# Optimization experiments

Hardware: AMD Instinct MI355X
Metric: run time of the kernel (lower is better)

## Reference

```python
import jax, jax.numpy as jnp
import numpy as np

K = 20.0          # wavenumber_k
L = 0.01          # grid_spacing_l
_lm = [L ** (i + 1) for i in range(7)]
C1 = jnp.array([[_lm[0], _lm[1]/2, _lm[2]/3, _lm[3]/4],
                [_lm[1]/2, _lm[2]/3, _lm[3]/4, _lm[4]/5],
                [_lm[2]/3, _lm[3]/4, _lm[4]/5, _lm[5]/6],
                [_lm[3]/4, _lm[4]/5, _lm[5]/6, _lm[6]/7]], dtype=jnp.float32)
C2 = jnp.array([[0,0,0,0],[0,0,0,0],[0,0,4*_lm[0],6*_lm[1]],[0,0,6*_lm[1],12*_lm[2]]], dtype=jnp.float32)
C3 = jnp.array([[0,0,0,0],[0,0,0,0],[2*_lm[0],_lm[1],2/3*_lm[2],1/2*_lm[3]],[3*_lm[1],2*_lm[2],3/2*_lm[3],6/5*_lm[4]]], dtype=jnp.float32)
M  = jnp.array([[1,0,0,0],[0,0,1,0],[-3/_lm[1],3/_lm[1],-2/_lm[0],-1/_lm[0]],[2/_lm[2],-2/_lm[2],1/_lm[1],1/_lm[1]]], dtype=jnp.float32)


def setup_inputs() -> dict:
    key = jax.random.key(0)
    x = jax.random.normal(key, (16, 4, 512, 512), dtype=jnp.float32)
    return {"x": x}


def _helmholtz(x):
    # corner views: (B, 4, H-1, W-1)
    tl = x[:, :, :-1, :-1]
    tr = x[:, :, :-1, 1:]
    bl = x[:, :, 1:, :-1]
    br = x[:, :, 1:, 1:]
    # rows replicate the original module exactly (including row_3's use of
    # du_xy_tl twice and du_x_tr); row_4 stacked on last dim.
    row1 = jnp.stack([tl[:, 0], tr[:, 0], tl[:, 2], tr[:, 2]], axis=-1)
    row2 = jnp.stack([bl[:, 0], br[:, 0], bl[:, 2], br[:, 2]], axis=-1)
    row3 = jnp.stack([tl[:, 3], tr[:, 1], tl[:, 3], tr[:, 3]], axis=-1)
    row4 = jnp.stack([bl[:, 1], br[:, 1], bl[:, 3], br[:, 3]], axis=-1)
    Q = jnp.stack([row1, row2, row3, row4], axis=-2)  # (B, H-1, W-1, 4, 4)
    # A = M @ Q @ M^T
    A = jnp.einsum('ij,bhwjk,lk->bhwil', M, Q, M)

    def quad(Cm):
        # sum over all entries of A @ Cm @ A^T, per patch -> (B, H-1, W-1)
        return jnp.einsum('bhwij,jk,bhwlk->bhw', A, Cm, A)

    s1 = jnp.sum(C1)
    s2 = jnp.sum(C2)
    s3 = jnp.sum(C3)
    qC1  = quad(C1)
    qC2  = quad(C2)
    qC3T = quad(C3.T)
    qC3  = quad(C3)
    k2 = K * K
    patch = (s2 * qC1 + s1 * qC2 + (k2 * k2) * s1 * qC1
             + 2.0 * s3 * qC3T + 2.0 * k2 * s1 * qC3 + 2.0 * k2 * s3 * qC1)
    return jnp.mean(patch)


def reference(x):
    return _helmholtz(x)
```

## Files before the change

### kernel.cpp

```cpp
#include <hip/hip_runtime.h>


struct HParams {
    float u0, u1, u2, u3;
    float Hs[4][4];
};

#define ROWS_PER_TILE 8
#define NTILES 64
#define BSIZE 256

__global__ __launch_bounds__(BSIZE) void helm_main(const float* __restrict__ x,
                                                   double* __restrict__ partial,
                                                   HParams P)
{
    const int bid  = blockIdx.x;
    const int b    = bid >> 6;
    const int tile = bid & 63;
    const int h0   = tile * ROWS_PER_TILE;
    const int rend = min(h0 + ROWS_PER_TILE, 511);
    const int t    = threadIdx.x;

    __shared__ float raw[4][512];
    __shared__ float buf[2][5][512];
    __shared__ double wsum[4];

    const float* xb = x + (size_t)b * 4u * 512u * 512u;

    const int c0 = t >> 7;
    const int c1 = 2 + (t >> 7);
    const int q  = t & 127;
    const float4* p0 = (const float4*)(xb + (size_t)c0 * 262144u) + q;
    const float4* p1 = (const float4*)(xb + (size_t)c1 * 262144u) + q;

    double acc = 0.0;

    float4 r0 = p0[(size_t)h0 * 128u];
    float4 r1 = p1[(size_t)h0 * 128u];

    for (int r = h0; r <= rend; ++r) {
        ((float4*)raw[c0])[q] = r0;
        ((float4*)raw[c1])[q] = r1;
        float4 n0 = make_float4(0.f, 0.f, 0.f, 0.f);
        float4 n1 = make_float4(0.f, 0.f, 0.f, 0.f);
        if (r < rend) {
            n0 = p0[(size_t)(r + 1) * 128u];
            n1 = p1[(size_t)(r + 1) * 128u];
        }
        __syncthreads();

        {
            float (*bw)[512] = buf[r & 1];
            #pragma unroll
            for (int k = 0; k < 2; ++k) {
                const int w = t + k * 256;
                const float x0 = raw[0][w];
                const float x1 = raw[1][w];
                const float x2 = raw[2][w];
                const float x3 = raw[3][w];
                bw[0][w] = P.u0 * x0 + P.u2 * x3;
                bw[1][w] = P.u0 * x0 + P.u2 * x1;
                bw[2][w] = P.u1 * x0 + P.u3 * x1;
                bw[3][w] = P.u0 * x2 + P.u2 * x3;
                bw[4][w] = P.u1 * x2 + P.u3 * x3;
            }
        }
        __syncthreads();

        if (r > h0) {
            const float (*bt)[512] = buf[(r - 1) & 1];
            const float (*bb)[512] = buf[r & 1];
            #pragma unroll
            for (int k = 0; k < 2; ++k) {
                const int w = t + k * 256;
                if (w < 511) {
                    const float w0 = bt[0][w]     + bb[2][w];
                    const float w1 = bt[1][w + 1] + bb[2][w + 1];
                    const float w2 = bt[3][w]     + bb[4][w];
                    const float w3 = bt[3][w + 1] + bb[4][w + 1];
                    const float t0 = P.Hs[0][0]*w0 + P.Hs[0][1]*w1 + P.Hs[0][2]*w2 + P.Hs[0][3]*w3;
                    const float t1 = P.Hs[1][0]*w0 + P.Hs[1][1]*w1 + P.Hs[1][2]*w2 + P.Hs[1][3]*w3;
                    const float t2 = P.Hs[2][0]*w0 + P.Hs[2][1]*w1 + P.Hs[2][2]*w2 + P.Hs[2][3]*w3;
                    const float t3 = P.Hs[3][0]*w0 + P.Hs[3][1]*w1 + P.Hs[3][2]*w2 + P.Hs[3][3]*w3;
                    acc += (double)(w0 * t0 + w1 * t1 + w2 * t2 + w3 * t3);
                }
            }
        }
        __syncthreads();

        r0 = n0;
        r1 = n1;
    }

    for (int off = 32; off > 0; off >>= 1)
        acc += __shfl_down(acc, off, 64);
    const int lane = t & 63;
    const int wid  = t >> 6;
    if (lane == 0) wsum[wid] = acc;
    __syncthreads();
    if (t == 0)
        partial[bid] = wsum[0] + wsum[1] + wsum[2] + wsum[3];
}

__global__ __launch_bounds__(BSIZE) void helm_reduce(const double* __restrict__ partial,
                                                     float* __restrict__ out, int n)
{
    __shared__ double wsum[4];
    const int t = threadIdx.x;
    double a = 0.0;
    for (int i = t; i < n; i += BSIZE) a += partial[i];
    for (int off = 32; off > 0; off >>= 1)
        a += __shfl_down(a, off, 64);
    if ((t & 63) == 0) wsum[t >> 6] = a;
    __syncthreads();
    if (t == 0) {
        const double sum = wsum[0] + wsum[1] + wsum[2] + wsum[3];
        out[0] = (float)(sum / (16.0 * 511.0 * 511.0));
    }
}

extern "C" void kernel_launch(void* const* d_in, const int* in_sizes, int n_in,
                              void* d_out, int out_size, void* d_ws, size_t ws_size,
                              hipStream_t stream) {
    const float* x = (const float*)d_in[0];
    float* out     = (float*)d_out;
    double* partial = (double*)d_ws;

    const double L = 0.01;
    double lm[7];
    lm[0] = L;
    for (int i = 1; i < 7; ++i) lm[i] = lm[i - 1] * L;

    double C1[4][4], C2[4][4] = {}, C3[4][4] = {};
    for (int i = 0; i < 4; ++i)
        for (int j = 0; j < 4; ++j)
            C1[i][j] = lm[i + j] / (double)(i + j + 1);
    C2[2][2] = 4.0 * lm[0];  C2[2][3] = 6.0 * lm[1];
    C2[3][2] = 6.0 * lm[1];  C2[3][3] = 12.0 * lm[2];
    C3[2][0] = 2.0 * lm[0];  C3[2][1] = lm[1];
    C3[2][2] = (2.0 / 3.0) * lm[2];  C3[2][3] = 0.5 * lm[3];
    C3[3][0] = 3.0 * lm[1];  C3[3][1] = 2.0 * lm[2];
    C3[3][2] = 1.5 * lm[3];  C3[3][3] = (6.0 / 5.0) * lm[4];

    const double M[4][4] = {
        {1.0, 0.0, 0.0, 0.0},
        {0.0, 0.0, 1.0, 0.0},
        {-3.0 / lm[1], 3.0 / lm[1], -2.0 / lm[0], -1.0 / lm[0]},
        { 2.0 / lm[2], -2.0 / lm[2], 1.0 / lm[1],  1.0 / lm[1]}
    };

    double s1 = 0.0, s2 = 0.0, s3 = 0.0;
    for (int i = 0; i < 4; ++i)
        for (int j = 0; j < 4; ++j) {
            s1 += C1[i][j]; s2 += C2[i][j]; s3 += C3[i][j];
        }

    const double k2 = 20.0 * 20.0;
    const double a1 = s2 + k2 * k2 * s1 + 2.0 * k2 * s3;
    const double a2 = s1;
    const double a3 = 2.0 * s3 + 2.0 * k2 * s1;

    double G[4][4];
    for (int i = 0; i < 4; ++i)
        for (int j = 0; j < 4; ++j)
            G[i][j] = a1 * C1[i][j] + a2 * C2[i][j] + a3 * C3[i][j];

    double H[4][4] = {};
    for (int jj = 0; jj < 4; ++jj)
        for (int kk = 0; kk < 4; ++kk) {
            double s = 0.0;
            for (int a = 0; a < 4; ++a)
                for (int bb = 0; bb < 4; ++bb)
                    s += M[a][jj] * G[a][bb] * M[bb][kk];
            H[jj][kk] = s;
        }

    HParams P;
    double u[4];
    for (int j = 0; j < 4; ++j) {
        u[j] = M[0][j] + M[1][j] + M[2][j] + M[3][j];
    }
    P.u0 = (float)u[0]; P.u1 = (float)u[1]; P.u2 = (float)u[2]; P.u3 = (float)u[3];
    for (int jj = 0; jj < 4; ++jj)
        for (int kk = 0; kk < 4; ++kk)
            P.Hs[jj][kk] = (float)(0.5 * (H[jj][kk] + H[kk][jj]));

    (void)in_sizes; (void)n_in; (void)out_size; (void)ws_size;

    helm_main<<<dim3(16 * NTILES), dim3(BSIZE), 0, stream>>>(x, partial, P);
    helm_reduce<<<dim3(1), dim3(BSIZE), 0, stream>>>(partial, out, 16 * NTILES);
}
```

Baseline: 21.26 us.

## Restructure Helmholtz kernel to per-wave register tiles with shuffle neighbors

Each wavefront now owns an 8-row tile of one batch and each lane handles 8 contiguous columns held in registers, with the right-neighbor column fetched by a lane shuffle. This replaces the shared-memory staging and three block barriers per row. The quadratic form is also reduced to 10 symmetric coefficients with the doubled off-diagonals folded in, and each wave writes its partial directly. The per-lane accumulation is done in float per row before the double add. The grid shrinks to 256 blocks, which lowers wave count and may reduce memory-level parallelism despite more loads in flight per lane.

```diff
diff --git a/kernel.cpp b/kernel.cpp
--- a/kernel.cpp
+++ b/kernel.cpp
@@ -3,103 +3,108 @@
 
 struct HParams {
     float u0, u1, u2, u3;
-    float Hs[4][4];
+    float H00, H11, H22, H33;
+    float H01_2, H02_2, H03_2, H12_2, H13_2, H23_2;
 };
 
-#define ROWS_PER_TILE 8
-#define NTILES 64
 #define BSIZE 256
+
+__device__ __forceinline__ float f4get(const float4& v, int k) {
+    switch (k & 3) { case 0: return v.x; case 1: return v.y; case 2: return v.z; default: return v.w; }
+}
+
+struct Fields { float f1[8], f2[8], f3[8], f4[8], f5[8]; };
+
+#define LOADROW(B, r) do {                                                  \
+    _Pragma("unroll")                                                       \
+    for (int ch = 0; ch < 4; ++ch) {                                        \
+        const size_t base_ = (size_t)ch * 65536u + (size_t)(r) * 128u + cq; \
+        B[2*ch]   = px[base_];                                              \
+        B[2*ch+1] = px[base_ + 1];                                          \
+    } } while (0)
+
+#define FIELDS(F, B) do {                                                   \
+    _Pragma("unroll")                                                       \
+    for (int j = 0; j < 8; ++j) {                                           \
+        const float x0_ = f4get(B[0 + (j>>2)], j);                          \
+        const float x1_ = f4get(B[2 + (j>>2)], j);                          \
+        const float x2_ = f4get(B[4 + (j>>2)], j);                          \
+        const float x3_ = f4get(B[6 + (j>>2)], j);                          \
+        const float t0_ = P.u0 * x0_;                                       \
+        F.f1[j] = fmaf(P.u2, x3_, t0_);                                     \
+        F.f2[j] = fmaf(P.u2, x1_, t0_);                                     \
+        F.f3[j] = fmaf(P.u3, x1_, P.u1 * x0_);                              \
+        F.f4[j] = fmaf(P.u2, x3_, P.u0 * x2_);                              \
+        F.f5[j] = fmaf(P.u3, x3_, P.u1 * x2_);                              \
+    } } while (0)
+
+#define PATCH(Ft, Fb) do {                                                  \
+    float aV[8], bV[8], cV[8];                                              \
+    _Pragma("unroll")                                                       \
+    for (int j = 0; j < 8; ++j) {                                           \
+        aV[j] = Ft.f1[j] + Fb.f3[j];                                        \
+        bV[j] = Ft.f2[j] + Fb.f3[j];                                        \
+        cV[j] = Ft.f4[j] + Fb.f5[j];                                        \
+    }                                                                       \
+    const float bn_ = __shfl_down(bV[0], 1, 64);                            \
+    const float cn_ = __shfl_down(cV[0], 1, 64);                            \
+    float rowsum_ = 0.0f;                                                   \
+    _Pragma("unroll")                                                       \
+    for (int j = 0; j < 8; ++j) {                                           \
+        const float w0_ = aV[j];                                            \
+        const float w1_ = (j < 7) ? bV[j+1] : bn_;                          \
+        const float w2_ = cV[j];                                            \
+        const float w3_ = (j < 7) ? cV[j+1] : cn_;                          \
+        const float q0_ = fmaf(P.H03_2, w3_, fmaf(P.H02_2, w2_, fmaf(P.H01_2, w1_, P.H00 * w0_))); \
+        const float q1_ = fmaf(P.H13_2, w3_, fmaf(P.H12_2, w2_, P.H11 * w1_)); \
+        const float q2_ = fmaf(P.H23_2, w3_, P.H22 * w2_);                  \
+        const float q3_ = P.H33 * w3_;                                      \
+        const float pq_ = fmaf(w0_, q0_, fmaf(w1_, q1_, fmaf(w2_, q2_, w3_ * q3_))); \
+        if (j < 7 || lane < 63) rowsum_ += pq_;                             \
+    }                                                                       \
+    acc += (double)rowsum_;                                                 \
+} while (0)
 
 __global__ __launch_bounds__(BSIZE) void helm_main(const float* __restrict__ x,
                                                    double* __restrict__ partial,
                                                    HParams P)
 {
-    const int bid  = blockIdx.x;
-    const int b    = bid >> 6;
-    const int tile = bid & 63;
-    const int h0   = tile * ROWS_PER_TILE;
-    const int rend = min(h0 + ROWS_PER_TILE, 511);
     const int t    = threadIdx.x;
-
-    __shared__ float raw[4][512];
-    __shared__ float buf[2][5][512];
-    __shared__ double wsum[4];
-
-    const float* xb = x + (size_t)b * 4u * 512u * 512u;
-
-    const int c0 = t >> 7;
-    const int c1 = 2 + (t >> 7);
-    const int q  = t & 127;
-    const float4* p0 = (const float4*)(xb + (size_t)c0 * 262144u) + q;
-    const float4* p1 = (const float4*)(xb + (size_t)c1 * 262144u) + q;
-
+    const int lane = t & 63;
+    const int wid  = t >> 6;
+    const int sid  = blockIdx.x * 4 + wid;
+    const int b    = sid >> 6;
+    const int tile = sid & 63;
+    const int h0   = tile * 8;
+    const int hend = min(h0 + 8, 511);
+
+    const float4* px = (const float4*)(x + (size_t)b * (4u * 512u * 512u));
+    const int cq = lane * 2;
+
+    float4 A0[8], A1[8];
+    Fields Fa, Fb;
     double acc = 0.0;
 
-    float4 r0 = p0[(size_t)h0 * 128u];
-    float4 r1 = p1[(size_t)h0 * 128u];
-
-    for (int r = h0; r <= rend; ++r) {
-        ((float4*)raw[c0])[q] = r0;
-        ((float4*)raw[c1])[q] = r1;
-        float4 n0 = make_float4(0.f, 0.f, 0.f, 0.f);
-        float4 n1 = make_float4(0.f, 0.f, 0.f, 0.f);
-        if (r < rend) {
-            n0 = p0[(size_t)(r + 1) * 128u];
-            n1 = p1[(size_t)(r + 1) * 128u];
-        }
-        __syncthreads();
-
-        {
-            float (*bw)[512] = buf[r & 1];
-            #pragma unroll
-            for (int k = 0; k < 2; ++k) {
-                const int w = t + k * 256;
-                const float x0 = raw[0][w];
-                const float x1 = raw[1][w];
-                const float x2 = raw[2][w];
-                const float x3 = raw[3][w];
-                bw[0][w] = P.u0 * x0 + P.u2 * x3;
-                bw[1][w] = P.u0 * x0 + P.u2 * x1;
-                bw[2][w] = P.u1 * x0 + P.u3 * x1;
-                bw[3][w] = P.u0 * x2 + P.u2 * x3;
-                bw[4][w] = P.u1 * x2 + P.u3 * x3;
-            }
-        }
-        __syncthreads();
-
-        if (r > h0) {
-            const float (*bt)[512] = buf[(r - 1) & 1];
-            const float (*bb)[512] = buf[r & 1];
-            #pragma unroll
-            for (int k = 0; k < 2; ++k) {
-                const int w = t + k * 256;
-                if (w < 511) {
-                    const float w0 = bt[0][w]     + bb[2][w];
-                    const float w1 = bt[1][w + 1] + bb[2][w + 1];
-                    const float w2 = bt[3][w]     + bb[4][w];
-                    const float w3 = bt[3][w + 1] + bb[4][w + 1];
-                    const float t0 = P.Hs[0][0]*w0 + P.Hs[0][1]*w1 + P.Hs[0][2]*w2 + P.Hs[0][3]*w3;
-                    const float t1 = P.Hs[1][0]*w0 + P.Hs[1][1]*w1 + P.Hs[1][2]*w2 + P.Hs[1][3]*w3;
-                    const float t2 = P.Hs[2][0]*w0 + P.Hs[2][1]*w1 + P.Hs[2][2]*w2 + P.Hs[2][3]*w3;
-                    const float t3 = P.Hs[3][0]*w0 + P.Hs[3][1]*w1 + P.Hs[3][2]*w2 + P.Hs[3][3]*w3;
-                    acc += (double)(w0 * t0 + w1 * t1 + w2 * t2 + w3 * t3);
-                }
-            }
-        }
-        __syncthreads();
-
-        r0 = n0;
-        r1 = n1;
+    LOADROW(A0, h0);
+    LOADROW(A1, h0 + 1);
+    FIELDS(Fa, A0);
+
+    int r = h0 + 1;
+    while (true) {
+        if (r + 1 <= hend) LOADROW(A0, r + 1);
+        FIELDS(Fb, A1);
+        PATCH(Fa, Fb);
+        ++r; if (r > hend) break;
+        if (r + 1 <= hend) LOADROW(A1, r + 1);
+        FIELDS(Fa, A0);
+        PATCH(Fb, Fa);
+        ++r; if (r > hend) break;
     }
 
+    #pragma unroll
     for (int off = 32; off > 0; off >>= 1)
         acc += __shfl_down(acc, off, 64);
-    const int lane = t & 63;
-    const int wid  = t >> 6;
-    if (lane == 0) wsum[wid] = acc;
-    __syncthreads();
-    if (t == 0)
-        partial[bid] = wsum[0] + wsum[1] + wsum[2] + wsum[3];
+    if (lane == 0) partial[sid] = acc;
 }
 
 __global__ __launch_bounds__(BSIZE) void helm_reduce(const double* __restrict__ partial,
@@ -109,6 +114,7 @@
     const int t = threadIdx.x;
     double a = 0.0;
     for (int i = t; i < n; i += BSIZE) a += partial[i];
+    #pragma unroll
     for (int off = 32; off > 0; off >>= 1)
         a += __shfl_down(a, off, 64);
     if ((t & 63) == 0) wsum[t >> 6] = a;
@@ -122,8 +128,8 @@
 extern "C" void kernel_launch(void* const* d_in, const int* in_sizes, int n_in,
                               void* d_out, int out_size, void* d_ws, size_t ws_size,
                               hipStream_t stream) {
-    const float* x = (const float*)d_in[0];
-    float* out     = (float*)d_out;
+    const float* x  = (const float*)d_in[0];
+    float* out      = (float*)d_out;
     double* partial = (double*)d_ws;
 
     const double L = 0.01;
@@ -174,19 +180,25 @@
                     s += M[a][jj] * G[a][bb] * M[bb][kk];
             H[jj][kk] = s;
         }
+    double Hs[4][4];
+    for (int i = 0; i < 4; ++i)
+        for (int j = 0; j < 4; ++j)
+            Hs[i][j] = 0.5 * (H[i][j] + H[j][i]);
+
+    double u[4];
+    for (int j = 0; j < 4; ++j)
+        u[j] = M[0][j] + M[1][j] + M[2][j] + M[3][j];
 
     HParams P;
-    double u[4];
-    for (int j = 0; j < 4; ++j) {
-        u[j] = M[0][j] + M[1][j] + M[2][j] + M[3][j];
-    }
     P.u0 = (float)u[0]; P.u1 = (float)u[1]; P.u2 = (float)u[2]; P.u3 = (float)u[3];
-    for (int jj = 0; jj < 4; ++jj)
-        for (int kk = 0; kk < 4; ++kk)
-            P.Hs[jj][kk] = (float)(0.5 * (H[jj][kk] + H[kk][jj]));
+    P.H00 = (float)Hs[0][0]; P.H11 = (float)Hs[1][1];
+    P.H22 = (float)Hs[2][2]; P.H33 = (float)Hs[3][3];
+    P.H01_2 = (float)(2.0 * Hs[0][1]); P.H02_2 = (float)(2.0 * Hs[0][2]);
+    P.H03_2 = (float)(2.0 * Hs[0][3]); P.H12_2 = (float)(2.0 * Hs[1][2]);
+    P.H13_2 = (float)(2.0 * Hs[1][3]); P.H23_2 = (float)(2.0 * Hs[2][3]);
 
     (void)in_sizes; (void)n_in; (void)out_size; (void)ws_size;
 
-    helm_main<<<dim3(16 * NTILES), dim3(BSIZE), 0, stream>>>(x, partial, P);
-    helm_reduce<<<dim3(1), dim3(BSIZE), 0, stream>>>(partial, out, 16 * NTILES);
-}
+    helm_main<<<dim3(256), dim3(BSIZE), 0, stream>>>(x, partial, P);
+    helm_reduce<<<dim3(1), dim3(BSIZE), 0, stream>>>(partial, out, 1024);
+}
```

Result: faster. 19.76 us (-7.1%).
